# Kernel optimization log

Measured on AMD Instinct MI355X. Metric: run time of the kernel, lower is better.

Reference implementation:

```python
import jax, jax.numpy as jnp
import numpy as np

N, E, D, G, OUT, K = 150000, 1200000, 128, 512, 2, 2
EPS = 1e-5


def setup_inputs() -> dict:
    key = jax.random.key(0)
    ks = jax.random.split(key, 8)
    nfeat = jax.random.normal(ks[0], (N, D), dtype=jnp.float32)
    src = jax.random.randint(ks[1], (E,), 0, N, dtype=jnp.int32)
    dst = jax.random.randint(ks[2], (E,), 0, N, dtype=jnp.int32)
    node2graph = jnp.sort(jax.random.randint(ks[3], (N,), 0, G, dtype=jnp.int32))
    s = 1.0 / np.sqrt(D)
    conv_w = jax.random.normal(ks[4], (D, D), dtype=jnp.float32) * s
    conv_b = jnp.zeros((D,), jnp.float32)
    gamma1 = jnp.ones((D,), jnp.float32)
    beta1 = jnp.zeros((D,), jnp.float32)
    gamma2 = jnp.ones((D,), jnp.float32)
    beta2 = jnp.zeros((D,), jnp.float32)
    pred_w = jax.random.normal(ks[5], (D, OUT), dtype=jnp.float32) * s
    pred_b = jnp.zeros((OUT,), jnp.float32)
    return {"nfeat": nfeat, "src": src, "dst": dst, "node2graph": node2graph,
            "num_graphs": G,
            "conv_w": conv_w, "conv_b": conv_b,
            "gamma1": gamma1, "beta1": beta1,
            "gamma2": gamma2, "beta2": beta2,
            "pred_w": pred_w, "pred_b": pred_b}


def _batchnorm(h, gamma, beta):
    # batch-norm over the node dimension (training-mode stats)
    mu = jnp.mean(h, axis=0)
    var = jnp.mean(jnp.square(h - mu), axis=0)
    return (h - mu) * jax.lax.rsqrt(var + EPS) * gamma + beta


def reference(nfeat, src, dst, node2graph, num_graphs,
              conv_w, conv_b, gamma1, beta1, gamma2, beta2, pred_w, pred_b):
    n = nfeat.shape[0]
    # symmetric degree normalization D^{-1/2} A D^{-1/2}
    deg = jax.ops.segment_sum(jnp.ones_like(dst, dtype=nfeat.dtype), dst, num_segments=n)
    dnorm = jax.lax.rsqrt(jnp.clip(deg, 1.0, None))  # [N]
    h = nfeat  # dropout with p=0 is identity
    for _ in range(K):  # k-hop SGC propagation interleaved with norm
        m = (h * dnorm[:, None])[src]                       # [E, D] gather
        h = jax.ops.segment_sum(m, dst, num_segments=n)     # scatter-add
        h = h * dnorm[:, None]
        h = _batchnorm(h, gamma1, beta1)
    h = h @ conv_w + conv_b          # SGConv linear
    h = _batchnorm(h, gamma2, beta2)  # middle norm
    h = jax.nn.relu(h)                # activation (dropout p=0)
    # mean pooling per graph
    cnt = jax.ops.segment_sum(jnp.ones((n,), h.dtype), node2graph, num_segments=num_graphs)
    g = jax.ops.segment_sum(h, node2graph, num_segments=num_graphs)
    g = g / jnp.clip(cnt, 1.0, None)[:, None]
    return g @ pred_w + pred_b  # [G, OUT]
```

## Files before the change

### kernel.cpp

```cpp
#include <hip/hip_runtime.h>
#include <hip/hip_fp16.h>
#include <cstddef>
#include <cstdint>

constexpr int DIMS = 128;
constexpr float BN_EPS = 1e-5f;
constexpr int NSH = 64;
constexpr int GB = 4096;
constexpr int NPB = 512;

typedef _Float16 f16x8 __attribute__((ext_vector_type(8)));
typedef float f32x4 __attribute__((ext_vector_type(4)));

static __device__ __forceinline__ f16x8 as_f16x8(uint4 u) {
  union { uint4 u; f16x8 h; } x; x.u = u; return x.h;
}
static __device__ __forceinline__ __half2 as_h2(uint32_t u) {
  union { uint32_t u; __half2 h; } x; x.u = u; return x.h;
}
static __device__ __forceinline__ uint32_t h2bits(__half2 h) {
  union { __half2 h; uint32_t u; } x; x.h = h; return x.u;
}

__global__ void zero_k(float* __restrict__ fp, size_t nf) {
  size_t i = (size_t)blockIdx.x * blockDim.x + threadIdx.x;
  if (i < nf) fp[i] = 0.f;
}

__global__ void cvt_k(const float4* __restrict__ in4, uint2* __restrict__ out,
                      const float* __restrict__ dnorm, size_t n32) {
  size_t i = (size_t)blockIdx.x * blockDim.x + threadIdx.x;
  size_t stride = (size_t)gridDim.x * blockDim.x;
  for (; i < n32; i += stride) {
    float d = dnorm[i >> 5];
    float4 v = in4[i];
    __half2 h0 = __floats2half2_rn(v.x * d, v.y * d);
    __half2 h1 = __floats2half2_rn(v.z * d, v.w * d);
    out[i] = make_uint2(h2bits(h0), h2bits(h1));
  }
}


__global__ __launch_bounds__(256) void cnt_k(const int* __restrict__ dst,
                                             int* __restrict__ C, int e, int chunk) {
  __shared__ int hist[512];
  int b = blockIdx.x;
  for (int j = threadIdx.x; j < 512; j += 256) hist[j] = 0;
  __syncthreads();
  int i0 = b * chunk;
  int i1 = i0 + chunk; if (i1 > e) i1 = e;
  for (int i = i0 + threadIdx.x; i < i1; i += 256)
    atomicAdd(&hist[dst[i] >> 9], 1);
  __syncthreads();
  for (int j = threadIdx.x; j < 512; j += 256) C[b * 512 + j] = hist[j];
}

__global__ __launch_bounds__(512) void colscan_k(int* __restrict__ C, int* __restrict__ tot) {
  int j = blockIdx.x;
  int t = threadIdx.x;
  int v = C[t * 512 + j];
  __shared__ int lds[512];
  lds[t] = v; __syncthreads();
  for (int off = 1; off < 512; off <<= 1) {
    int add = (t >= off) ? lds[t - off] : 0;
    __syncthreads();
    lds[t] += add;
    __syncthreads();
  }
  C[t * 512 + j] = lds[t] - v;
  if (t == 511) tot[j] = lds[511];
}

__global__ __launch_bounds__(512) void bscan_k(const int* __restrict__ tot, int nbins,
                                               int* __restrict__ boff, int* __restrict__ adj,
                                               int e) {
  int t = threadIdx.x;
  int v = tot[t];
  __shared__ int lds[512];
  lds[t] = v; __syncthreads();
  for (int off = 1; off < 512; off <<= 1) {
    int add = (t >= off) ? lds[t - off] : 0;
    __syncthreads();
    lds[t] += add;
    __syncthreads();
  }
  boff[t] = lds[t] - v;
  if (t == 0) boff[nbins] = e;
  if (t < 16) adj[e + t] = 0;
}

__global__ __launch_bounds__(512) void scat_k(const int* __restrict__ src,
                                              const int* __restrict__ dst,
                                              const int* __restrict__ C,
                                              const int* __restrict__ boff,
                                              int* __restrict__ ebin, int e, int chunk) {
  __shared__ int cur[512];
  int b = blockIdx.x;
  int t = threadIdx.x;
  cur[t] = boff[t] + C[b * 512 + t];
  __syncthreads();
  int i0 = b * chunk;
  int i1 = i0 + chunk; if (i1 > e) i1 = e;
  for (int i = i0 + t; i < i1; i += 512) {
    int d = dst[i];
    int bin = d >> 9;
    int p = atomicAdd(&cur[bin], 1);
    ebin[p] = (src[i] << 9) | (d & 511);
  }
}

__global__ __launch_bounds__(512) void binidx_k(
    const int* __restrict__ ebin, const int* __restrict__ boff,
    int* __restrict__ row_off, float* __restrict__ dnorm, int n, int nbins) {
  __shared__ int cnt[512];
  __shared__ int scn[512];
  int b = blockIdx.x;
  int t = threadIdx.x;
  cnt[t] = 0;
  __syncthreads();
  int j0 = boff[b], j1 = boff[b + 1];
  for (int i = j0 + t; i < j1; i += 512) atomicAdd(&cnt[ebin[i] & 511], 1);
  __syncthreads();
  int v = cnt[t];
  scn[t] = v; __syncthreads();
  for (int off = 1; off < 512; off <<= 1) {
    int add = (t >= off) ? scn[t - off] : 0;
    __syncthreads();
    scn[t] += add;
    __syncthreads();
  }
  int node = (b << 9) + t;
  if (node < n) {
    row_off[node] = j0 + scn[t] - v;
    dnorm[node] = rsqrtf(fmaxf((float)v, 1.0f));
  }
  if (b == nbins - 1 && t == 0) row_off[n] = j1;
}

__global__ __launch_bounds__(512) void adj_bins_k(
    const int* __restrict__ ebin, const int* __restrict__ boff,
    const int* __restrict__ row_off, const float* __restrict__ dnorm,
    int* __restrict__ adj, float* __restrict__ wsum, int n) {
  __shared__ int cur[512];
  __shared__ int ro[512];
  __shared__ float ws[512];
  int b = blockIdx.x;
  int base = b << 9;
  int t = threadIdx.x;
  {
    cur[t] = 0;
    ws[t] = 0.f;
    int node = base + t;
    ro[t] = (node < n) ? row_off[node] : 0;
  }
  __syncthreads();
  int j0 = boff[b], j1 = boff[b + 1];
  for (int i = j0 + t; i < j1; i += 512) {
    int pk = ebin[i];
    int dl = pk & 511;
    int s = pk >> 9;
    int p = atomicAdd(&cur[dl], 1);
    adj[ro[dl] + p] = s;
    atomicAdd(&ws[dl], dnorm[s]);
  }
  __syncthreads();
  {
    int node = base + t;
    if (node < n) wsum[node] = ws[t];
  }
}

template <bool AFF, int PASS>
__global__ __launch_bounds__(256) void gather_k(
    const uint32_t* __restrict__ Xu, uint32_t* __restrict__ Yout,
    const int* __restrict__ row_off, const int* __restrict__ adj,
    const float* __restrict__ dn, const float* __restrict__ wsum,
    const float* __restrict__ a, const float* __restrict__ b,
    float* __restrict__ sumS, float* __restrict__ sqS, int n, int nwaves) {
  int tid = threadIdx.x;
  int l = tid & 63, w = tid >> 6;
  int wid = blockIdx.x * 4 + w;
  int lg = l >> 5;
  uint32_t fl = (uint32_t)(l & 31);
  const uint32_t XOFF = PASS * 32;
  int f0 = PASS * 64 + 2 * (int)fl;
  float af0 = 1.f, bf0 = 0.f, af1 = 1.f, bf1 = 0.f;
  if (AFF) { af0 = a[f0]; bf0 = b[f0]; af1 = a[f0 + 1]; bf1 = b[f0 + 1]; }
  float s0 = 0.f, s1 = 0.f, q0 = 0.f, q1 = 0.f;

  for (int nodeA = wid; nodeA < n; nodeA += 2 * nwaves) {
    const int nodeB = nodeA + nwaves;
    const bool hasB = nodeB < n;
    int ja = row_off[nodeA];
    const int ea = row_off[nodeA + 1];
    int jb = hasB ? row_off[nodeB] : 0;
    const int eb = hasB ? row_off[nodeB + 1] : 0;
    float accA0 = 0.f, accA1 = 0.f, accB0 = 0.f, accB1 = 0.f;

    while ((ja < ea) || (jb < eb)) {
      uint32_t xa[8], xb[8];
      const bool runA = ja < ea, runB = jb < eb;
      if (runA) {
#pragma unroll
        for (int t = 0; t < 8; ++t) {
          int jj = ja + 2 * t + lg;
          int jc = jj < ea ? jj : ea - 1;
          uint32_t sj = (uint32_t)adj[jc];
          uint32_t v = Xu[(sj << 6) + XOFF + fl];
          xa[t] = (jj < ea) ? v : 0u;
        }
      }
      if (runB) {
#pragma unroll
        for (int t = 0; t < 8; ++t) {
          int jj = jb + 2 * t + lg;
          int jc = jj < eb ? jj : eb - 1;
          uint32_t sj = (uint32_t)adj[jc];
          uint32_t v = Xu[(sj << 6) + XOFF + fl];
          xb[t] = (jj < eb) ? v : 0u;
        }
      }
      if (runA) {
        __half2 t0 = __hadd2(as_h2(xa[0]), as_h2(xa[1]));
        __half2 t1 = __hadd2(as_h2(xa[2]), as_h2(xa[3]));
        __half2 t2 = __hadd2(as_h2(xa[4]), as_h2(xa[5]));
        __half2 t3 = __hadd2(as_h2(xa[6]), as_h2(xa[7]));
        float2 u0 = __half22float2(__hadd2(t0, t1));
        float2 u1 = __half22float2(__hadd2(t2, t3));
        accA0 += u0.x + u1.x;
        accA1 += u0.y + u1.y;
        ja += 16;
      }
      if (runB) {
        __half2 t0 = __hadd2(as_h2(xb[0]), as_h2(xb[1]));
        __half2 t1 = __hadd2(as_h2(xb[2]), as_h2(xb[3]));
        __half2 t2 = __hadd2(as_h2(xb[4]), as_h2(xb[5]));
        __half2 t3 = __hadd2(as_h2(xb[6]), as_h2(xb[7]));
        float2 u0 = __half22float2(__hadd2(t0, t1));
        float2 u1 = __half22float2(__hadd2(t2, t3));
        accB0 += u0.x + u1.x;
        accB1 += u0.y + u1.y;
        jb += 16;
      }
    }

    accA0 += __shfl_xor(accA0, 32);
    accA1 += __shfl_xor(accA1, 32);
    if (hasB) {
      accB0 += __shfl_xor(accB0, 32);
      accB1 += __shfl_xor(accB1, 32);
    }

    {
      float dnn = dn[nodeA];
      float v0, v1;
      if constexpr (AFF) {
        float wsn = wsum[nodeA];
        v0 = dnn * fmaf(af0, accA0, bf0 * wsn);
        v1 = dnn * fmaf(af1, accA1, bf1 * wsn);
        if (lg == 0)
          Yout[((uint32_t)nodeA << 6) + XOFF + fl] = h2bits(__floats2half2_rn(v0, v1));
      } else {
        v0 = dnn * accA0;
        v1 = dnn * accA1;
        if (lg == 0)
          Yout[((uint32_t)nodeA << 6) + XOFF + fl] =
              h2bits(__floats2half2_rn(v0 * dnn, v1 * dnn));
      }
      s0 += v0; s1 += v1; q0 += v0 * v0; q1 += v1 * v1;
    }
    if (hasB) {
      float dnn = dn[nodeB];
      float v0, v1;
      if constexpr (AFF) {
        float wsn = wsum[nodeB];
        v0 = dnn * fmaf(af0, accB0, bf0 * wsn);
        v1 = dnn * fmaf(af1, accB1, bf1 * wsn);
        if (lg == 0)
          Yout[((uint32_t)nodeB << 6) + XOFF + fl] = h2bits(__floats2half2_rn(v0, v1));
      } else {
        v0 = dnn * accB0;
        v1 = dnn * accB1;
        if (lg == 0)
          Yout[((uint32_t)nodeB << 6) + XOFF + fl] =
              h2bits(__floats2half2_rn(v0 * dnn, v1 * dnn));
      }
      s0 += v0; s1 += v1; q0 += v0 * v0; q1 += v1 * v1;
    }
  }

  __shared__ float red[4][128];
  if (lg == 0) {
    red[w][0 * 32 + fl] = s0;
    red[w][1 * 32 + fl] = s1;
    red[w][2 * 32 + fl] = q0;
    red[w][3 * 32 + fl] = q1;
  }
  __syncthreads();
  if (tid < 128) {
    float v = red[0][tid] + red[1][tid] + red[2][tid] + red[3][tid];
    int comp = tid >> 5, fs = tid & 31;
    int f = PASS * 64 + 2 * fs + (comp & 1);
    float* dstp = (comp & 2) ? sqS : sumS;
    int sh = blockIdx.x & (NSH - 1);
    atomicAdd(&dstp[sh * DIMS + f], v);
  }
}

__global__ void affine_k(const float* __restrict__ sum, const float* __restrict__ sq,
                         const float* __restrict__ gamma, const float* __restrict__ beta,
                         float* __restrict__ a, float* __restrict__ b, float invn) {
  int d = threadIdx.x;
  float s = 0.f, q = 0.f;
  for (int k = 0; k < NSH; ++k) { s += sum[k * DIMS + d]; q += sq[k * DIMS + d]; }
  float mu = s * invn;
  float var = q * invn - mu * mu;
  float rs = rsqrtf(var + BN_EPS);
  float ad = rs * gamma[d];
  a[d] = ad;
  b[d] = beta[d] - mu * ad;
}

__global__ void foldw_k(const float* __restrict__ W, const float* __restrict__ cb,
                        const float* __restrict__ a2, const float* __restrict__ b2,
                        __half* __restrict__ Wt, float* __restrict__ cp) {
  int o = blockIdx.x;
  int d = threadIdx.x;
  float w = W[d * DIMS + o];
  Wt[o * DIMS + d] = __float2half(a2[d] * w);
  __shared__ float red[128];
  red[d] = b2[d] * w;
  __syncthreads();
  for (int off = 64; off > 0; off >>= 1) {
    if (d < off) red[d] += red[d + off];
    __syncthreads();
  }
  if (d == 0) cp[o] = red[0] + cb[o];
}

__global__ __launch_bounds__(256) void matmul_k(
    const uint4* __restrict__ X, const uint4* __restrict__ Wt,
    const float* __restrict__ cp, uint4* __restrict__ Z,
    float* __restrict__ sumS, float* __restrict__ sqS, int n) {
  int tid = threadIdx.x;
  int l = tid & 63, w = tid >> 6;
  int rowg = l & 15;
  int kg = l >> 4;
  int r0 = (blockIdx.x * 4 + w) * 32;
  bool active = r0 < n;

  __shared__ __half outs[4][16][136];
  __shared__ float sred[4][128], qred[4][128];
  float svals[8], qvals[8];

  if (active) {
    f32x4 acc0[8] = {}, acc1[8] = {};
    const uint4* xr0 = X + (size_t)(r0 + rowg) * 16;
    const uint4* xr1 = X + (size_t)(r0 + 16 + rowg) * 16;
    bool ok0 = (r0 + rowg) < n;
    bool ok1 = (r0 + 16 + rowg) < n;
#pragma unroll
    for (int kk = 0; kk < 4; ++kk) {
      uint4 au0 = ok0 ? xr0[kk * 4 + kg] : make_uint4(0u, 0u, 0u, 0u);
      uint4 au1 = ok1 ? xr1[kk * 4 + kg] : make_uint4(0u, 0u, 0u, 0u);
      f16x8 a0 = as_f16x8(au0), a1 = as_f16x8(au1);
#pragma unroll
      for (int c = 0; c < 8; ++c) {
        f16x8 bfr = as_f16x8(Wt[(size_t)(c * 16 + rowg) * 16 + kk * 4 + kg]);
        acc0[c] = __builtin_amdgcn_mfma_f32_16x16x32_f16(a0, bfr, acc0[c], 0, 0, 0);
        acc1[c] = __builtin_amdgcn_mfma_f32_16x16x32_f16(a1, bfr, acc1[c], 0, 0, 0);
      }
    }
#pragma unroll
    for (int c = 0; c < 8; ++c) { svals[c] = 0.f; qvals[c] = 0.f; }
#pragma unroll
    for (int gidx = 0; gidx < 2; ++gidx) {
      int rbase = r0 + gidx * 16;
#pragma unroll
      for (int c = 0; c < 8; ++c) {
        float cpv = cp[c * 16 + rowg];
        f32x4 av = (gidx == 0) ? acc0[c] : acc1[c];
#pragma unroll
        for (int r = 0; r < 4; ++r) {
          int row = rbase + kg * 4 + r;
          float vv = av[r] + cpv;
          vv = (row < n) ? vv : 0.f;
          svals[c] += vv; qvals[c] += vv * vv;
          outs[w][kg * 4 + r][c * 16 + rowg] = __float2half(vv);
        }
      }
#pragma unroll
      for (int it = 0; it < 4; ++it) {
        int lr = it * 4 + kg;
        int grow = rbase + lr;
        if (grow < n)
          Z[(size_t)grow * 16 + rowg] = *(const uint4*)&outs[w][lr][rowg * 8];
      }
    }
#pragma unroll
    for (int c = 0; c < 8; ++c) {
      svals[c] += __shfl_xor(svals[c], 16); svals[c] += __shfl_xor(svals[c], 32);
      qvals[c] += __shfl_xor(qvals[c], 16); qvals[c] += __shfl_xor(qvals[c], 32);
    }
  }
  if (active) {
    if (kg == 0) {
#pragma unroll
      for (int c = 0; c < 8; ++c) {
        sred[w][c * 16 + rowg] = svals[c];
        qred[w][c * 16 + rowg] = qvals[c];
      }
    }
  } else {
    sred[w][l] = 0.f; sred[w][64 + l] = 0.f;
    qred[w][l] = 0.f; qred[w][64 + l] = 0.f;
  }
  __syncthreads();
  int f = tid & 127;
  int sh = blockIdx.x & (NSH - 1);
  if (tid < 128) {
    float s = sred[0][f] + sred[1][f] + sred[2][f] + sred[3][f];
    atomicAdd(&sumS[sh * DIMS + f], s);
  } else {
    float q = qred[0][f] + qred[1][f] + qred[2][f] + qred[3][f];
    atomicAdd(&sqS[sh * DIMS + f], q);
  }
}

__global__ void gstart_k(const int* __restrict__ n2g, int* __restrict__ gstart, int n, int G) {
  int i = blockIdx.x * blockDim.x + threadIdx.x;
  if (i >= n) return;
  int g = n2g[i];
  int gp = (i == 0) ? -1 : n2g[i - 1];
  for (int x = gp + 1; x <= g; ++x) gstart[x] = i;
  if (i == n - 1) {
    for (int x = g + 1; x <= G; ++x) gstart[x] = n;
  }
}

__global__ __launch_bounds__(512) void pool_pred_k(
    const uint4* __restrict__ Z, const int* __restrict__ gstart,
    const float* __restrict__ a3, const float* __restrict__ b3,
    const float* __restrict__ pw, const float* __restrict__ pb,
    float* __restrict__ out) {
  int g = blockIdx.x;
  int tid = threadIdx.x;
  int l = tid & 63, w = tid >> 6;
  int grp = l >> 4, fl = l & 15;
  int f0 = fl * 8;
  float av[8], bv[8];
#pragma unroll
  for (int q = 0; q < 8; ++q) { av[q] = a3[f0 + q]; bv[q] = b3[f0 + q]; }
  int s = gstart[g], e = gstart[g + 1];
  float rs[8] = {0.f, 0.f, 0.f, 0.f, 0.f, 0.f, 0.f, 0.f};
  for (int ni = s + (w * 4 + grp); ni < e; ni += 32) {
    uint4 zv = Z[(size_t)ni * 16 + fl];
    const __half2* h = (const __half2*)&zv;
#pragma unroll
    for (int q = 0; q < 4; ++q) {
      float2 z = __half22float2(h[q]);
      rs[2 * q] += fmaxf(fmaf(z.x, av[2 * q], bv[2 * q]), 0.f);
      rs[2 * q + 1] += fmaxf(fmaf(z.y, av[2 * q + 1], bv[2 * q + 1]), 0.f);
    }
  }
  float p0 = 0.f, p1 = 0.f;
#pragma unroll
  for (int q = 0; q < 8; ++q) {
    p0 += rs[q] * pw[(f0 + q) * 2 + 0];
    p1 += rs[q] * pw[(f0 + q) * 2 + 1];
  }
  __shared__ float r[2][512];
  r[0][tid] = p0; r[1][tid] = p1;
  __syncthreads();
  for (int off = 256; off > 0; off >>= 1) {
    if (tid < off) { r[0][tid] += r[0][tid + off]; r[1][tid] += r[1][tid + off]; }
    __syncthreads();
  }
  if (tid == 0) {
    float inv = 1.f / fmaxf((float)(e - s), 1.f);
    out[g * 2 + 0] = r[0][0] * inv + pb[0];
    out[g * 2 + 1] = r[1][0] * inv + pb[1];
  }
}

extern "C" void kernel_launch(void* const* d_in, const int* in_sizes, int n_in,
                              void* d_out, int out_size, void* d_ws, size_t ws_size,
                              hipStream_t stream) {
  const float* nfeat  = (const float*)d_in[0];
  const int*   src    = (const int*)d_in[1];
  const int*   dst    = (const int*)d_in[2];
  const int*   n2g    = (const int*)d_in[3];
  const float* conv_w = (const float*)d_in[5];
  const float* conv_b = (const float*)d_in[6];
  const float* gamma1 = (const float*)d_in[7];
  const float* beta1  = (const float*)d_in[8];
  const float* gamma2 = (const float*)d_in[9];
  const float* beta2  = (const float*)d_in[10];
  const float* pred_w = (const float*)d_in[11];
  const float* pred_b = (const float*)d_in[12];
  float* out = (float*)d_out;
  (void)n_in; (void)ws_size;

  const int n = in_sizes[0] / DIMS;
  const int e = in_sizes[1];
  const int g = out_size / 2;
  const int nbins = (n + 511) >> 9;

  char* p = (char*)d_ws;
  auto alloc = [&](size_t bytes) { char* r = p; p += (bytes + 255) & ~(size_t)255; return r; };
  uint32_t* Xp  = (uint32_t*)alloc((size_t)n * 64 * 4);
  uint32_t* W1  = (uint32_t*)alloc((size_t)n * 64 * 4);
  uint32_t* Y2  = (uint32_t*)alloc((size_t)n * 64 * 4);
  __half*   Zh  = (__half*)alloc((size_t)n * 64 * 4);
  float* dnorm = (float*)alloc((size_t)n * 4);
  float* stat  = (float*)alloc(((size_t)6 * NSH * DIMS + n) * 4);
  float* wsum  = stat + 6 * NSH * DIMS;
  float* affA  = (float*)alloc(3 * DIMS * 4);
  float* affB  = (float*)alloc(3 * DIMS * 4);
  __half* Wt   = (__half*)alloc(DIMS * DIMS * 2);
  float* cp    = (float*)alloc(DIMS * 4);
  int* row_off = (int*)alloc(((size_t)n + 1) * 4);
  int* adj     = (int*)alloc(((size_t)e + 16) * 4);
  int* ebin    = (int*)alloc((size_t)e * 4);
  int* Cmat    = (int*)alloc((size_t)NPB * 512 * 4);
  int* tot     = (int*)alloc(512 * 4);
  int* boff    = (int*)alloc(520 * 4);
  int* gstart  = (int*)alloc(((size_t)g + 1) * 4);

  const int SLAB = NSH * DIMS;
  float* S0 = stat + 0 * SLAB; float* Q0 = stat + 1 * SLAB;
  float* S1 = stat + 2 * SLAB; float* Q1 = stat + 3 * SLAB;
  float* S2 = stat + 4 * SLAB; float* Q2 = stat + 5 * SLAB;

  const float invn = 1.0f / (float)n;
  const int nwaves = GB * 4;
  const int chunk = (e + NPB - 1) / NPB;

  zero_k<<<dim3(((size_t)6 * SLAB + 255) / 256), dim3(256), 0, stream>>>(stat, (size_t)6 * SLAB);
  cnt_k<<<dim3(NPB), dim3(256), 0, stream>>>(dst, Cmat, e, chunk);
  colscan_k<<<dim3(512), dim3(512), 0, stream>>>(Cmat, tot);
  bscan_k<<<dim3(1), dim3(512), 0, stream>>>(tot, nbins, boff, adj, e);
  scat_k<<<dim3(NPB), dim3(512), 0, stream>>>(src, dst, Cmat, boff, ebin, e, chunk);
  binidx_k<<<dim3(nbins), dim3(512), 0, stream>>>(ebin, boff, row_off, dnorm, n, nbins);
  cvt_k<<<dim3(2048), dim3(256), 0, stream>>>((const float4*)nfeat, (uint2*)Xp, dnorm,
                                              (size_t)n * 32);
  adj_bins_k<<<dim3(nbins), dim3(512), 0, stream>>>(ebin, boff, row_off, dnorm, adj, wsum, n);

  gather_k<false, 0><<<dim3(GB), dim3(256), 0, stream>>>(
      Xp, W1, row_off, adj, dnorm, wsum, nullptr, nullptr, S0, Q0, n, nwaves);
  gather_k<false, 1><<<dim3(GB), dim3(256), 0, stream>>>(
      Xp, W1, row_off, adj, dnorm, wsum, nullptr, nullptr, S0, Q0, n, nwaves);
  affine_k<<<dim3(1), dim3(DIMS), 0, stream>>>(S0, Q0, gamma1, beta1, affA + 0, affB + 0, invn);
  gather_k<true, 0><<<dim3(GB), dim3(256), 0, stream>>>(
      W1, Y2, row_off, adj, dnorm, wsum, affA + 0, affB + 0, S1, Q1, n, nwaves);
  gather_k<true, 1><<<dim3(GB), dim3(256), 0, stream>>>(
      W1, Y2, row_off, adj, dnorm, wsum, affA + 0, affB + 0, S1, Q1, n, nwaves);
  affine_k<<<dim3(1), dim3(DIMS), 0, stream>>>(S1, Q1, gamma1, beta1, affA + DIMS, affB + DIMS, invn);
  foldw_k<<<dim3(DIMS), dim3(DIMS), 0, stream>>>(conv_w, conv_b, affA + DIMS, affB + DIMS, Wt, cp);
  matmul_k<<<dim3((n + 127) / 128), dim3(256), 0, stream>>>(
      (const uint4*)Y2, (const uint4*)Wt, cp, (uint4*)Zh, S2, Q2, n);
  affine_k<<<dim3(1), dim3(DIMS), 0, stream>>>(S2, Q2, gamma2, beta2, affA + 2 * DIMS, affB + 2 * DIMS, invn);
  gstart_k<<<dim3((n + 255) / 256), dim3(256), 0, stream>>>(n2g, gstart, n, g);
  pool_pred_k<<<dim3(g), dim3(512), 0, stream>>>((const uint4*)Zh, gstart,
                                                 affA + 2 * DIMS, affB + 2 * DIMS,
                                                 pred_w, pred_b, out);
}
```

Baseline: 293.4 us.

## Slice feature matrix into 8 column slabs and gather one slab per launch

```diff
diff --git a/kernel.cpp b/kernel.cpp
--- a/kernel.cpp
+++ b/kernel.cpp
@@ -6,7 +6,7 @@
 constexpr int DIMS = 128;
 constexpr float BN_EPS = 1e-5f;
 constexpr int NSH = 64;
-constexpr int GB = 4096;
+constexpr int GB2 = 2048;
 constexpr int NPB = 512;
 
 typedef _Float16 f16x8 __attribute__((ext_vector_type(8)));
@@ -27,16 +27,18 @@
   if (i < nf) fp[i] = 0.f;
 }
 
-__global__ void cvt_k(const float4* __restrict__ in4, uint2* __restrict__ out,
-                      const float* __restrict__ dnorm, size_t n32) {
+__global__ void cvt_k(const float2* __restrict__ in2, uint32_t* __restrict__ out,
+                      const float* __restrict__ dnorm, int n) {
+  size_t total = (size_t)n * 64;
   size_t i = (size_t)blockIdx.x * blockDim.x + threadIdx.x;
   size_t stride = (size_t)gridDim.x * blockDim.x;
-  for (; i < n32; i += stride) {
-    float d = dnorm[i >> 5];
-    float4 v = in4[i];
-    __half2 h0 = __floats2half2_rn(v.x * d, v.y * d);
-    __half2 h1 = __floats2half2_rn(v.z * d, v.w * d);
-    out[i] = make_uint2(h2bits(h0), h2bits(h1));
+  for (; i < total; i += stride) {
+    int nd = (int)(i >> 6);
+    int wg = (int)(i & 63);
+    float d = dnorm[nd];
+    float2 v = in2[i];
+    out[((size_t)(wg >> 3) * n + nd) * 8 + (wg & 7)] =
+        h2bits(__floats2half2_rn(v.x * d, v.y * d));
   }
 }
 
@@ -170,20 +172,20 @@
   }
 }
 
-template <bool AFF, int PASS>
+template <bool AFF>
 __global__ __launch_bounds__(256) void gather_k(
     const uint32_t* __restrict__ Xu, uint32_t* __restrict__ Yout,
     const int* __restrict__ row_off, const int* __restrict__ adj,
     const float* __restrict__ dn, const float* __restrict__ wsum,
     const float* __restrict__ a, const float* __restrict__ b,
-    float* __restrict__ sumS, float* __restrict__ sqS, int n, int nwaves) {
+    float* __restrict__ sumS, float* __restrict__ sqS, int n, int nwaves, int slice) {
   int tid = threadIdx.x;
   int l = tid & 63, w = tid >> 6;
   int wid = blockIdx.x * 4 + w;
-  int lg = l >> 5;
-  uint32_t fl = (uint32_t)(l & 31);
-  const uint32_t XOFF = PASS * 32;
-  int f0 = PASS * 64 + 2 * (int)fl;
+  int es = l >> 3;
+  uint32_t wl = (uint32_t)(l & 7);
+  const size_t SBASE = (size_t)slice * n;
+  int f0 = slice * 16 + 2 * (int)wl;
   float af0 = 1.f, bf0 = 0.f, af1 = 1.f, bf1 = 0.f;
   if (AFF) { af0 = a[f0]; bf0 = b[f0]; af1 = a[f0 + 1]; bf1 = b[f0 + 1]; }
   float s0 = 0.f, s1 = 0.f, q0 = 0.f, q1 = 0.f;
@@ -198,57 +200,45 @@
     float accA0 = 0.f, accA1 = 0.f, accB0 = 0.f, accB1 = 0.f;
 
     while ((ja < ea) || (jb < eb)) {
-      uint32_t xa[8], xb[8];
+      uint32_t xa[2], xb[2];
       const bool runA = ja < ea, runB = jb < eb;
       if (runA) {
 #pragma unroll
-        for (int t = 0; t < 8; ++t) {
-          int jj = ja + 2 * t + lg;
+        for (int t2 = 0; t2 < 2; ++t2) {
+          int jj = ja + 8 * t2 + es;
           int jc = jj < ea ? jj : ea - 1;
           uint32_t sj = (uint32_t)adj[jc];
-          uint32_t v = Xu[(sj << 6) + XOFF + fl];
-          xa[t] = (jj < ea) ? v : 0u;
+          uint32_t v = Xu[(SBASE + sj) * 8 + wl];
+          xa[t2] = (jj < ea) ? v : 0u;
         }
       }
       if (runB) {
 #pragma unroll
-        for (int t = 0; t < 8; ++t) {
-          int jj = jb + 2 * t + lg;
+        for (int t2 = 0; t2 < 2; ++t2) {
+          int jj = jb + 8 * t2 + es;
           int jc = jj < eb ? jj : eb - 1;
           uint32_t sj = (uint32_t)adj[jc];
-          uint32_t v = Xu[(sj << 6) + XOFF + fl];
-          xb[t] = (jj < eb) ? v : 0u;
+          uint32_t v = Xu[(SBASE + sj) * 8 + wl];
+          xb[t2] = (jj < eb) ? v : 0u;
         }
       }
       if (runA) {
-        __half2 t0 = __hadd2(as_h2(xa[0]), as_h2(xa[1]));
-        __half2 t1 = __hadd2(as_h2(xa[2]), as_h2(xa[3]));
-        __half2 t2 = __hadd2(as_h2(xa[4]), as_h2(xa[5]));
-        __half2 t3 = __hadd2(as_h2(xa[6]), as_h2(xa[7]));
-        float2 u0 = __half22float2(__hadd2(t0, t1));
-        float2 u1 = __half22float2(__hadd2(t2, t3));
-        accA0 += u0.x + u1.x;
-        accA1 += u0.y + u1.y;
+        float2 u = __half22float2(__hadd2(as_h2(xa[0]), as_h2(xa[1])));
+        accA0 += u.x; accA1 += u.y;
         ja += 16;
       }
       if (runB) {
-        __half2 t0 = __hadd2(as_h2(xb[0]), as_h2(xb[1]));
-        __half2 t1 = __hadd2(as_h2(xb[2]), as_h2(xb[3]));
-        __half2 t2 = __hadd2(as_h2(xb[4]), as_h2(xb[5]));
-        __half2 t3 = __hadd2(as_h2(xb[6]), as_h2(xb[7]));
-        float2 u0 = __half22float2(__hadd2(t0, t1));
-        float2 u1 = __half22float2(__hadd2(t2, t3));
-        accB0 += u0.x + u1.x;
-        accB1 += u0.y + u1.y;
+        float2 u = __half22float2(__hadd2(as_h2(xb[0]), as_h2(xb[1])));
+        accB0 += u.x; accB1 += u.y;
         jb += 16;
       }
     }
 
-    accA0 += __shfl_xor(accA0, 32);
-    accA1 += __shfl_xor(accA1, 32);
+    accA0 += __shfl_xor(accA0, 8);  accA0 += __shfl_xor(accA0, 16); accA0 += __shfl_xor(accA0, 32);
+    accA1 += __shfl_xor(accA1, 8);  accA1 += __shfl_xor(accA1, 16); accA1 += __shfl_xor(accA1, 32);
     if (hasB) {
-      accB0 += __shfl_xor(accB0, 32);
-      accB1 += __shfl_xor(accB1, 32);
+      accB0 += __shfl_xor(accB0, 8);  accB0 += __shfl_xor(accB0, 16); accB0 += __shfl_xor(accB0, 32);
+      accB1 += __shfl_xor(accB1, 8);  accB1 += __shfl_xor(accB1, 16); accB1 += __shfl_xor(accB1, 32);
     }
 
     {
@@ -258,14 +248,13 @@
         float wsn = wsum[nodeA];
         v0 = dnn * fmaf(af0, accA0, bf0 * wsn);
         v1 = dnn * fmaf(af1, accA1, bf1 * wsn);
-        if (lg == 0)
-          Yout[((uint32_t)nodeA << 6) + XOFF + fl] = h2bits(__floats2half2_rn(v0, v1));
+        if (es == 0)
+          Yout[(SBASE + nodeA) * 8 + wl] = h2bits(__floats2half2_rn(v0, v1));
       } else {
         v0 = dnn * accA0;
         v1 = dnn * accA1;
-        if (lg == 0)
-          Yout[((uint32_t)nodeA << 6) + XOFF + fl] =
-              h2bits(__floats2half2_rn(v0 * dnn, v1 * dnn));
+        if (es == 0)
+          Yout[(SBASE + nodeA) * 8 + wl] = h2bits(__floats2half2_rn(v0 * dnn, v1 * dnn));
       }
       s0 += v0; s1 += v1; q0 += v0 * v0; q1 += v1 * v1;
     }
@@ -276,34 +265,32 @@
         float wsn = wsum[nodeB];
         v0 = dnn * fmaf(af0, accB0, bf0 * wsn);
         v1 = dnn * fmaf(af1, accB1, bf1 * wsn);
-        if (lg == 0)
-          Yout[((uint32_t)nodeB << 6) + XOFF + fl] = h2bits(__floats2half2_rn(v0, v1));
+        if (es == 0)
+          Yout[(SBASE + nodeB) * 8 + wl] = h2bits(__floats2half2_rn(v0, v1));
       } else {
         v0 = dnn * accB0;
         v1 = dnn * accB1;
-        if (lg == 0)
-          Yout[((uint32_t)nodeB << 6) + XOFF + fl] =
-              h2bits(__floats2half2_rn(v0 * dnn, v1 * dnn));
+        if (es == 0)
+          Yout[(SBASE + nodeB) * 8 + wl] = h2bits(__floats2half2_rn(v0 * dnn, v1 * dnn));
       }
       s0 += v0; s1 += v1; q0 += v0 * v0; q1 += v1 * v1;
     }
   }
 
-  __shared__ float red[4][128];
-  if (lg == 0) {
-    red[w][0 * 32 + fl] = s0;
-    red[w][1 * 32 + fl] = s1;
-    red[w][2 * 32 + fl] = q0;
-    red[w][3 * 32 + fl] = q1;
-  }
-  __syncthreads();
-  if (tid < 128) {
+  __shared__ float red[4][32];
+  if (es == 0) {
+    red[w][0 * 8 + wl] = s0;
+    red[w][1 * 8 + wl] = s1;
+    red[w][2 * 8 + wl] = q0;
+    red[w][3 * 8 + wl] = q1;
+  }
+  __syncthreads();
+  if (tid < 32) {
     float v = red[0][tid] + red[1][tid] + red[2][tid] + red[3][tid];
-    int comp = tid >> 5, fs = tid & 31;
-    int f = PASS * 64 + 2 * fs + (comp & 1);
+    int comp = tid >> 3, ws2 = tid & 7;
+    int f = slice * 16 + 2 * ws2 + (comp & 1);
     float* dstp = (comp & 2) ? sqS : sumS;
-    int sh = blockIdx.x & (NSH - 1);
-    atomicAdd(&dstp[sh * DIMS + f], v);
+    atomicAdd(&dstp[(blockIdx.x & (NSH - 1)) * DIMS + f], v);
   }
 }
 
@@ -355,14 +342,17 @@
 
   if (active) {
     f32x4 acc0[8] = {}, acc1[8] = {};
-    const uint4* xr0 = X + (size_t)(r0 + rowg) * 16;
-    const uint4* xr1 = X + (size_t)(r0 + 16 + rowg) * 16;
-    bool ok0 = (r0 + rowg) < n;
-    bool ok1 = (r0 + 16 + rowg) < n;
+    int row0 = r0 + rowg, row1 = r0 + 16 + rowg;
+    bool ok0 = row0 < n;
+    bool ok1 = row1 < n;
 #pragma unroll
     for (int kk = 0; kk < 4; ++kk) {
-      uint4 au0 = ok0 ? xr0[kk * 4 + kg] : make_uint4(0u, 0u, 0u, 0u);
-      uint4 au1 = ok1 ? xr1[kk * 4 + kg] : make_uint4(0u, 0u, 0u, 0u);
+#pragma unroll
+      for (int dummy = 0; dummy < 1; ++dummy) {}
+      int u = kk * 4 + kg;
+      size_t base = ((size_t)(u >> 1) * n) * 2 + (u & 1);
+      uint4 au0 = ok0 ? X[base + (size_t)row0 * 2] : make_uint4(0u, 0u, 0u, 0u);
+      uint4 au1 = ok1 ? X[base + (size_t)row1 * 2] : make_uint4(0u, 0u, 0u, 0u);
       f16x8 a0 = as_f16x8(au0), a1 = as_f16x8(au1);
 #pragma unroll
       for (int c = 0; c < 8; ++c) {
@@ -533,7 +523,7 @@
   float* S2 = stat + 4 * SLAB; float* Q2 = stat + 5 * SLAB;
 
   const float invn = 1.0f / (float)n;
-  const int nwaves = GB * 4;
+  const int nwaves = GB2 * 4;
   const int chunk = (e + NPB - 1) / NPB;
 
   zero_k<<<dim3(((size_t)6 * SLAB + 255) / 256), dim3(256), 0, stream>>>(stat, (size_t)6 * SLAB);
@@ -542,19 +532,16 @@
   bscan_k<<<dim3(1), dim3(512), 0, stream>>>(tot, nbins, boff, adj, e);
   scat_k<<<dim3(NPB), dim3(512), 0, stream>>>(src, dst, Cmat, boff, ebin, e, chunk);
   binidx_k<<<dim3(nbins), dim3(512), 0, stream>>>(ebin, boff, row_off, dnorm, n, nbins);
-  cvt_k<<<dim3(2048), dim3(256), 0, stream>>>((const float4*)nfeat, (uint2*)Xp, dnorm,
-                                              (size_t)n * 32);
+  cvt_k<<<dim3(2048), dim3(256), 0, stream>>>((const float2*)nfeat, Xp, dnorm, n);
   adj_bins_k<<<dim3(nbins), dim3(512), 0, stream>>>(ebin, boff, row_off, dnorm, adj, wsum, n);
 
-  gather_k<false, 0><<<dim3(GB), dim3(256), 0, stream>>>(
-      Xp, W1, row_off, adj, dnorm, wsum, nullptr, nullptr, S0, Q0, n, nwaves);
-  gather_k<false, 1><<<dim3(GB), dim3(256), 0, stream>>>(
-      Xp, W1, row_off, adj, dnorm, wsum, nullptr, nullptr, S0, Q0, n, nwaves);
+  for (int s = 0; s < 8; ++s)
+    gather_k<false><<<dim3(GB2), dim3(256), 0, stream>>>(
+        Xp, W1, row_off, adj, dnorm, wsum, nullptr, nullptr, S0, Q0, n, nwaves, s);
   affine_k<<<dim3(1), dim3(DIMS), 0, stream>>>(S0, Q0, gamma1, beta1, affA + 0, affB + 0, invn);
-  gather_k<true, 0><<<dim3(GB), dim3(256), 0, stream>>>(
-      W1, Y2, row_off, adj, dnorm, wsum, affA + 0, affB + 0, S1, Q1, n, nwaves);
-  gather_k<true, 1><<<dim3(GB), dim3(256), 0, stream>>>(
-      W1, Y2, row_off, adj, dnorm, wsum, affA + 0, affB + 0, S1, Q1, n, nwaves);
+  for (int s = 0; s < 8; ++s)
+    gather_k<true><<<dim3(GB2), dim3(256), 0, stream>>>(
+        W1, Y2, row_off, adj, dnorm, wsum, affA + 0, affB + 0, S1, Q1, n, nwaves, s);
   affine_k<<<dim3(1), dim3(DIMS), 0, stream>>>(S1, Q1, gamma1, beta1, affA + DIMS, affB + DIMS, invn);
   foldw_k<<<dim3(DIMS), dim3(DIMS), 0, stream>>>(conv_w, conv_b, affA + DIMS, affB + DIMS, Wt, cp);
   matmul_k<<<dim3((n + 127) / 128), dim3(256), 0, stream>>>(
```

Result: slower. 665.8 us (+126.9%).
